# Performance work log

Hardware: AMD Instinct MI355X
Metric: run time of the kernel (lower is better)

The kernel has to match this reference:

```python
import jax, jax.numpy as jnp
import numpy as np

B, T, H, NH = 16, 2048, 1024, 16
HD = H // NH  # 64
IN0, IN1 = 256, 512  # modality input sizes needing projection; modality 2 is already H


def _ln(x, g, b, eps=1e-5):
    m = jnp.mean(x, axis=-1, keepdims=True)
    v = jnp.mean((x - m) ** 2, axis=-1, keepdims=True)
    return (x - m) / jnp.sqrt(v + eps) * g + b


def setup_inputs() -> dict:
    key = jax.random.key(0)
    ks = jax.random.split(key, 24)
    s = 0.02
    d = {
        'x0': jax.random.normal(ks[0], (B, T, IN0), jnp.float32),
        'x1': jax.random.normal(ks[1], (B, T, IN1), jnp.float32),
        'x2': jax.random.normal(ks[2], (B, T, H), jnp.float32),
        'static_context': jax.random.normal(ks[3], (B, T, H), jnp.float32),
        'Wp0': jax.random.normal(ks[4], (H, IN0), jnp.float32) * s,
        'bp0': jnp.zeros((H,), jnp.float32),
        'Wp1': jax.random.normal(ks[5], (H, IN1), jnp.float32) * s,
        'bp1': jnp.zeros((H,), jnp.float32),
        'Wq': jax.random.normal(ks[6], (H, H), jnp.float32) * s,
        'bq': jnp.zeros((H,), jnp.float32),
        'Wk': jax.random.normal(ks[7], (H, H), jnp.float32) * s,
        'bk': jnp.zeros((H,), jnp.float32),
        'Wv': jax.random.normal(ks[8], (H, H), jnp.float32) * s,
        'bv': jnp.zeros((H,), jnp.float32),
        'Wo': jax.random.normal(ks[9], (H, H), jnp.float32) * s,
        'bo': jnp.zeros((H,), jnp.float32),
        'query_token': jax.random.normal(ks[10], (H,), jnp.float32) * s,
        'g1': jnp.ones((H,), jnp.float32),
        'be1': jnp.zeros((H,), jnp.float32),
        'g2': jnp.ones((H,), jnp.float32),
        'be2': jnp.zeros((H,), jnp.float32),
        'W1': jax.random.normal(ks[11], (4 * H, H), jnp.float32) * s,
        'b1': jnp.zeros((4 * H,), jnp.float32),
        'W2': jax.random.normal(ks[12], (H, 4 * H), jnp.float32) * s,
        'b2': jnp.zeros((H,), jnp.float32),
    }
    return d


def _forward(x0, x1, x2, static_context, Wp0, bp0, Wp1, bp1, Wq, bq, Wk, bk, Wv, bv,
             Wo, bo, query_token, g1, be1, g2, be2, W1, b1, W2, b2):
    # project modalities to hidden size, stack -> [B, T, M, H]
    m0 = x0 @ Wp0.T + bp0
    m1 = x1 @ Wp1.T + bp1
    stacked = jnp.stack([m0, m1, x2], axis=2)  # [B,T,3,H]
    M = stacked.shape[2]
    # per-timestep single-query cross-attention over the M modality tokens,
    # batched over all B*T positions (equivalent to the torch per-t loop)
    q = query_token + static_context  # [B,T,H]
    Q = (q @ Wq.T + bq).reshape(B, T, NH, HD)
    K = (stacked @ Wk.T + bk).reshape(B, T, M, NH, HD)
    V = (stacked @ Wv.T + bv).reshape(B, T, M, NH, HD)
    scores = jnp.einsum('bthd,btmhd->bthm', Q, K) / jnp.sqrt(jnp.asarray(HD, Q.dtype))
    attn = jax.nn.softmax(scores, axis=-1)  # [B,T,NH,M]
    weights = attn.mean(axis=2)  # average over heads (torch default) -> [B,T,M]
    ctx = jnp.einsum('bthm,btmhd->bthd', attn, V).reshape(B, T, H)
    attn_out = ctx @ Wo.T + bo
    fused = _ln(attn_out, g1, be1)
    ff = jax.nn.gelu(fused @ W1.T + b1, approximate=False) @ W2.T + b2
    fused = _ln(fused + ff, g2, be2)
    return fused, weights


def reference(x0, x1, x2, static_context, Wp0, bp0, Wp1, bp1, Wq, bq, Wk, bk, Wv, bv,
              Wo, bo, query_token, g1, be1, g2, be2, W1, b1, W2, b2):
    return _forward(x0, x1, x2, static_context, Wp0, bp0, Wp1, bp1, Wq, bq, Wk, bk,
                    Wv, bv, Wo, bo, query_token, g1, be1, g2, be2, W1, b1, W2, b2)
```

## Files before the change

kernel.cpp:

```cpp
#include <hip/hip_runtime.h>
#include <hip/hip_bf16.h>
#include <math.h>

#define BT 32768
#define HH 1024

typedef unsigned short u16;
typedef __attribute__((ext_vector_type(4))) unsigned short u16x4;
typedef __attribute__((ext_vector_type(8))) __bf16 bf16x8;
typedef __attribute__((ext_vector_type(4))) float f32x4;

#define DEVI static __device__ __forceinline__

DEVI u16 f2bf(float f){
  unsigned u = __builtin_bit_cast(unsigned, f);
  u += 0x7FFFu + ((u >> 16) & 1u);
  return (u16)(u >> 16);
}
DEVI float bf2f(u16 h){
  unsigned u = ((unsigned)h) << 16;
  return __builtin_bit_cast(float, u);
}
DEVI void gl_lds16(const void* g, void* l){
  __builtin_amdgcn_global_load_lds((const __attribute__((address_space(1))) void*)g,
                                   (__attribute__((address_space(3))) void*)l, 16, 0, 0);
}
DEVI int swz(int row, int elem){ return elem ^ ((row & 7) << 3); }

__global__ void k_cast4(const float* __restrict__ s, u16* __restrict__ d, int n4){
  int i = blockIdx.x*blockDim.x + threadIdx.x;
  int st = gridDim.x*blockDim.x;
  for (; i < n4; i += st){
    float4 v = ((const float4*)s)[i];
    u16x4 o = { f2bf(v.x), f2bf(v.y), f2bf(v.z), f2bf(v.w) };
    ((u16x4*)d)[i] = o;
  }
}

__global__ void k_qb(const float* __restrict__ qt, const float* __restrict__ sc,
                     u16* __restrict__ d, int n4){
  int i = blockIdx.x*blockDim.x + threadIdx.x;
  int st = gridDim.x*blockDim.x;
  for (; i < n4; i += st){
    int e = i*4; int c = e & 1023;
    float4 v = *(const float4*)&sc[e];
    float4 q = *(const float4*)&qt[c];
    u16x4 o = { f2bf(v.x+q.x), f2bf(v.y+q.y), f2bf(v.z+q.z), f2bf(v.w+q.w) };
    ((u16x4*)d)[i] = o;
  }
}

__global__ void k_copyf(const float* __restrict__ s, float* __restrict__ d, int n){
  int i = blockIdx.x*blockDim.x + threadIdx.x;
  int st = gridDim.x*blockDim.x;
  for (; i < n; i += st) d[i] = s[i];
}

__global__ void k_transcast(const float* __restrict__ s, u16* __restrict__ d, int R, int C){
  __shared__ float tile[32][33];
  int c0 = blockIdx.x*32, r0 = blockIdx.y*32;
  int tx = threadIdx.x & 31, ty = threadIdx.x >> 5;
  #pragma unroll
  for (int i = 0; i < 32; i += 8) tile[ty+i][tx] = s[(size_t)(r0+ty+i)*C + c0+tx];
  __syncthreads();
  #pragma unroll
  for (int i = 0; i < 32; i += 8) d[(size_t)(c0+ty+i)*R + r0+tx] = f2bf(tile[tx][ty+i]);
}

__global__ void k_matvec(const u16* __restrict__ W, const float* __restrict__ x,
                         const float* __restrict__ badd, float* __restrict__ out, int K){
  int row = blockIdx.x*4 + (threadIdx.x>>6);
  int lane = threadIdx.x & 63;
  float s = 0.f;
  for (int k = lane; k < K; k += 64) s += bf2f(W[(size_t)row*K + k]) * x[k];
  #pragma unroll
  for (int m = 1; m < 64; m <<= 1) s += __shfl_xor(s, m);
  if (lane == 0) out[row] = s + badd[row];
}

__global__ __launch_bounds__(256, 3)
void k_gemm(const u16* __restrict__ A, int lda,
            const u16* __restrict__ B, int ldb, int K,
            const float* __restrict__ bias,
            u16* __restrict__ C, int ldc, int col0, int act)
{
  __shared__ u16 As[128*64];
  __shared__ u16 Bs[128*64];
  const int tid = threadIdx.x, lane = tid & 63, wid = tid >> 6;
  const int wr = wid >> 1, wc = wid & 1;
  const int r15 = lane & 15, g = lane >> 4;
  const int m0 = blockIdx.x * 128, n0 = blockIdx.y * 128;
  f32x4 acc[4][4] = {};

  for (int k0 = 0; k0 < K; k0 += 64){
    #pragma unroll
    for (int it = 0; it < 4; ++it){
      int c = it*256 + tid;
      int row = c >> 3;
      int ke = swz(row, (c & 7) * 8);
      gl_lds16(A + (size_t)(m0+row)*lda + (k0+ke), As + c*8);
      gl_lds16(B + (size_t)(n0+row)*ldb + (k0+ke), Bs + c*8);
    }
    __syncthreads();
    #pragma unroll
    for (int kk = 0; kk < 64; kk += 32){
      bf16x8 av[4], bvv[4];
      #pragma unroll
      for (int i = 0; i < 4; ++i){
        int row = wr*64 + i*16 + r15;
        av[i] = *(const bf16x8*)&As[row*64 + swz(row, kk + g*8)];
      }
      #pragma unroll
      for (int j = 0; j < 4; ++j){
        int row = wc*64 + j*16 + r15;
        bvv[j] = *(const bf16x8*)&Bs[row*64 + swz(row, kk + g*8)];
      }
      #pragma unroll
      for (int i = 0; i < 4; ++i)
        #pragma unroll
        for (int j = 0; j < 4; ++j)
          acc[i][j] = __builtin_amdgcn_mfma_f32_16x16x32_bf16(av[i], bvv[j], acc[i][j], 0, 0, 0);
    }
    __syncthreads();
  }
  #pragma unroll
  for (int j = 0; j < 4; ++j){
    int col = wc*64 + j*16 + r15;
    float bb = bias ? bias[n0 + col] : 0.f;
    #pragma unroll
    for (int i = 0; i < 4; ++i){
      #pragma unroll
      for (int jj = 0; jj < 4; ++jj){
        int row = wr*64 + i*16 + g*4 + jj;
        float v = acc[i][j][jj] + bb;
        if (act == 1) v = 0.5f * v * (1.f + erff(v * 0.70710678118654752f));
        C[(size_t)(m0+row)*ldc + col0 + n0 + col] = f2bf(v);
      }
    }
  }
}

__global__ __launch_bounds__(512, 2)
void k_gemm8(const u16* __restrict__ A, int lda,
             const u16* __restrict__ B, int ldb, int K,
             const float* __restrict__ bias,
             u16* __restrict__ C, int ldc, int act, int nn)
{
  __shared__ u16 As[2][2][128*64];
  __shared__ u16 Bs[2][2][128*64];
  const int tid = threadIdx.x, lane = tid & 63, wid = tid >> 6;
  const int wr = wid >> 2, wc = wid & 3;
  const int r15 = lane & 15, g = lane >> 4;
  const int cpx = gridDim.x >> 3;
  const int sid = ((int)blockIdx.x & 7) * cpx + ((int)blockIdx.x >> 3);
  const int m0 = (sid / nn) * 256, n0 = (sid % nn) * 256;
  const int nt = K >> 6;
  f32x4 acc[8][4] = {};
  const int srow = tid >> 3, scol = (tid & 7) * 8;

  auto stA = [&](int buf, int half, int t){
    int k0 = (t < nt ? t : nt-1) << 6;
    #pragma unroll
    for (int l = 0; l < 2; ++l){
      int lr = l*64 + srow;
      gl_lds16(A + (size_t)(m0 + half*128 + lr)*lda + k0 + swz(lr, scol),
               &As[buf][half][lr*64 + scol]);
    }
  };
  auto stB = [&](int buf, int half, int t){
    int k0 = (t < nt ? t : nt-1) << 6;
    #pragma unroll
    for (int l = 0; l < 2; ++l){
      int lr = l*64 + srow;
      gl_lds16(B + (size_t)(n0 + half*128 + lr)*ldb + k0 + swz(lr, scol),
               &Bs[buf][half][lr*64 + scol]);
    }
  };

  bf16x8 av[4][2], bv[2][2];
  auto loadq = [&](int buf, int MI, int NJ){
    #pragma unroll
    for (int i = 0; i < 4; ++i){
      int r = wr*64 + i*16 + r15;
      #pragma unroll
      for (int k2 = 0; k2 < 2; ++k2)
        av[i][k2] = *(const bf16x8*)&As[buf][MI][r*64 + swz(r, k2*32 + g*8)];
    }
    #pragma unroll
    for (int j = 0; j < 2; ++j){
      int cr = wc*32 + j*16 + r15;
      #pragma unroll
      for (int k2 = 0; k2 < 2; ++k2)
        bv[j][k2] = *(const bf16x8*)&Bs[buf][NJ][cr*64 + swz(cr, k2*32 + g*8)];
    }
  };
  auto mmaq = [&](int MI, int NJ){
    __builtin_amdgcn_s_setprio(1);
    #pragma unroll
    for (int k2 = 0; k2 < 2; ++k2)
      #pragma unroll
      for (int i = 0; i < 4; ++i)
        #pragma unroll
        for (int j = 0; j < 2; ++j)
          acc[MI*4+i][NJ*2+j] = __builtin_amdgcn_mfma_f32_16x16x32_bf16(
              av[i][k2], bv[j][k2], acc[MI*4+i][NJ*2+j], 0, 0, 0);
    __builtin_amdgcn_s_setprio(0);
  };

  stA(0,0,0); stA(0,1,0); stB(0,0,0); stB(0,1,0); stB(1,0,1); stA(1,0,1);
  asm volatile("s_waitcnt vmcnt(4)" ::: "memory");
  __builtin_amdgcn_s_barrier();

  for (int t = 0; t < nt; ++t){
    const int cur = t & 1, opp = cur ^ 1;
    loadq(cur, 0, 0);
    stA(opp, 1, t+1);
    mmaq(0, 0);
    asm volatile("s_waitcnt vmcnt(6) lgkmcnt(0)" ::: "memory");
    __builtin_amdgcn_s_barrier();
    loadq(cur, 1, 0);
    stB(opp, 1, t+1);
    mmaq(1, 0);
    asm volatile("s_waitcnt lgkmcnt(0)" ::: "memory");
    __builtin_amdgcn_s_barrier();
    loadq(cur, 0, 1);
    stB(cur, 0, t+2);
    mmaq(0, 1);
    asm volatile("s_waitcnt lgkmcnt(0)" ::: "memory");
    __builtin_amdgcn_s_barrier();
    loadq(cur, 1, 1);
    stA(cur, 0, t+2);
    mmaq(1, 1);
    asm volatile("s_waitcnt vmcnt(6) lgkmcnt(0)" ::: "memory");
    __builtin_amdgcn_s_barrier();
  }
  asm volatile("s_waitcnt vmcnt(0)" ::: "memory");

  #pragma unroll
  for (int jf = 0; jf < 4; ++jf){
    int col = n0 + (jf>>1)*128 + wc*32 + (jf&1)*16 + r15;
    float bb = bias ? bias[col] : 0.f;
    #pragma unroll
    for (int fi = 0; fi < 8; ++fi){
      #pragma unroll
      for (int jj = 0; jj < 4; ++jj){
        int row = m0 + (fi>>2)*128 + wr*64 + (fi&3)*16 + g*4 + jj;
        float v = acc[fi][jf][jj] + bb;
        if (act == 1) v = 0.5f * v * (1.f + erff(v * 0.70710678118654752f));
        C[(size_t)row*ldc + col] = f2bf(v);
      }
    }
  }
}

__global__ __launch_bounds__(512, 4)
void k_attn2p(const u16* __restrict__ x0b, const u16* __restrict__ x1b, const u16* __restrict__ x2b,
              const u16* __restrict__ Wc0, const u16* __restrict__ Wc1, const u16* __restrict__ Wc2,
              const float* __restrict__ bc0, const float* __restrict__ bc1, const float* __restrict__ bc2,
              const u16* __restrict__ Qg, u16* __restrict__ ctx, float* __restrict__ wacc)
{
  __shared__ __align__(16) u16 As[128*64];
  __shared__ __align__(16) u16 Bs[128*64];
  __shared__ float Sl[2*128*3];

  const int tid = threadIdx.x, lane = tid & 63, wid = tid >> 6;
  const int wr = wid >> 1, h = wid & 1;
  const int r15 = lane & 15, g = lane >> 4;
  const int bid = blockIdx.x;
  const int xcd = bid & 7;
  const int bn = (bid >> 3) & 7;
  const int btb = (bid >> 6) * 8 + xcd;
  const int t0 = btb * 128, n0 = bn * 128;

  const u16* Xs[3] = { x0b, x1b, x2b };
  const u16* Ws[3] = { Wc0, Wc1, Wc2 };
  const float* Bc[3] = { bc0, bc1, bc2 };
  const int Ks[3] = { 256, 512, 1024 };

  const int srow = tid >> 3;
  const int scol = (tid & 7) * 8;

  #pragma unroll
  for (int m = 0; m < 3; ++m){
    const int K = Ks[m];
    const u16* X = Xs[m];
    const u16* W = Ws[m];
    f32x4 aK[2][4] = {};
    for (int k0 = 0; k0 < K; k0 += 64){
      #pragma unroll
      for (int l = 0; l < 2; ++l){
        int row = l*64 + srow;
        int ke = swz(row, scol);
        gl_lds16(X + (size_t)(t0+row)*K + k0 + ke, &As[row*64 + scol]);
        gl_lds16(W + (size_t)(n0+row)*K + k0 + ke, &Bs[row*64 + scol]);
      }
      __syncthreads();
      #pragma unroll
      for (int kk = 0; kk < 64; kk += 32){
        bf16x8 av[2], bv[4];
        #pragma unroll
        for (int i = 0; i < 2; ++i){
          int ra = wr*32 + i*16 + r15;
          av[i] = *(const bf16x8*)&As[ra*64 + swz(ra, kk + g*8)];
        }
        #pragma unroll
        for (int j = 0; j < 4; ++j){
          int rb = h*64 + j*16 + r15;
          bv[j] = *(const bf16x8*)&Bs[rb*64 + swz(rb, kk + g*8)];
        }
        #pragma unroll
        for (int i = 0; i < 2; ++i)
          #pragma unroll
          for (int j = 0; j < 4; ++j)
            aK[i][j] = __builtin_amdgcn_mfma_f32_16x16x32_bf16(av[i], bv[j], aK[i][j], 0, 0, 0);
      }
      __syncthreads();
    }
    float bkc[4];
    #pragma unroll
    for (int j = 0; j < 4; ++j) bkc[j] = Bc[m][n0 + h*64 + j*16 + r15];
    #pragma unroll
    for (int i = 0; i < 2; ++i){
      #pragma unroll
      for (int jj = 0; jj < 4; ++jj){
        int tt = wr*32 + i*16 + g*4 + jj;
        const u16* qrow = Qg + (size_t)(t0+tt)*1024 + n0 + h*64 + r15;
        float s = 0.f;
        #pragma unroll
        for (int j = 0; j < 4; ++j)
          s += (aK[i][j][jj] + bkc[j]) * bf2f(qrow[j*16]);
        s += __shfl_xor(s, 1); s += __shfl_xor(s, 2);
        s += __shfl_xor(s, 4); s += __shfl_xor(s, 8);
        if (r15 == 0) Sl[(h*128 + tt)*3 + m] = s * 0.125f;
      }
    }
  }
  __syncthreads();
  if (tid < 256){
    int h2 = tid >> 7, tt = tid & 127;
    int base = (h2*128 + tt)*3;
    float s0 = Sl[base+0], s1 = Sl[base+1], s2 = Sl[base+2];
    float mx = fmaxf(s0, fmaxf(s1, s2));
    float e0 = expf(s0-mx), e1 = expf(s1-mx), e2 = expf(s2-mx);
    float inv = 1.f/(e0+e1+e2);
    e0 *= inv; e1 *= inv; e2 *= inv;
    Sl[base+0] = e0; Sl[base+1] = e1; Sl[base+2] = e2;
    atomicAdd(&wacc[(size_t)(t0+tt)*3 + 0], e0*0.0625f);
    atomicAdd(&wacc[(size_t)(t0+tt)*3 + 1], e1*0.0625f);
    atomicAdd(&wacc[(size_t)(t0+tt)*3 + 2], e2*0.0625f);
  }
  __syncthreads();

  f32x4 ctxa[2][4] = {};
  #pragma unroll
  for (int m = 0; m < 3; ++m){
    const int K = Ks[m];
    const u16* X = Xs[m];
    const u16* W = Ws[m] + (size_t)1024*K;
    f32x4 aV[2][4] = {};
    for (int k0 = 0; k0 < K; k0 += 64){
      #pragma unroll
      for (int l = 0; l < 2; ++l){
        int row = l*64 + srow;
        int ke = swz(row, scol);
        gl_lds16(X + (size_t)(t0+row)*K + k0 + ke, &As[row*64 + scol]);
        gl_lds16(W + (size_t)(n0+row)*K + k0 + ke, &Bs[row*64 + scol]);
      }
      __syncthreads();
      #pragma unroll
      for (int kk = 0; kk < 64; kk += 32){
        bf16x8 av[2], bv[4];
        #pragma unroll
        for (int i = 0; i < 2; ++i){
          int ra = wr*32 + i*16 + r15;
          av[i] = *(const bf16x8*)&As[ra*64 + swz(ra, kk + g*8)];
        }
        #pragma unroll
        for (int j = 0; j < 4; ++j){
          int rb = h*64 + j*16 + r15;
          bv[j] = *(const bf16x8*)&Bs[rb*64 + swz(rb, kk + g*8)];
        }
        #pragma unroll
        for (int i = 0; i < 2; ++i)
          #pragma unroll
          for (int j = 0; j < 4; ++j)
            aV[i][j] = __builtin_amdgcn_mfma_f32_16x16x32_bf16(av[i], bv[j], aV[i][j], 0, 0, 0);
      }
      __syncthreads();
    }
    #pragma unroll
    for (int j = 0; j < 4; ++j){
      float bvv = Bc[m][1024 + n0 + h*64 + j*16 + r15];
      #pragma unroll
      for (int i = 0; i < 2; ++i){
        #pragma unroll
        for (int jj = 0; jj < 4; ++jj){
          int tt = wr*32 + i*16 + g*4 + jj;
          float p = Sl[(h*128 + tt)*3 + m];
          ctxa[i][j][jj] += p * (aV[i][j][jj] + bvv);
        }
      }
    }
  }
  #pragma unroll
  for (int i = 0; i < 2; ++i){
    #pragma unroll
    for (int jj = 0; jj < 4; ++jj){
      int tt = wr*32 + i*16 + g*4 + jj;
      #pragma unroll
      for (int j = 0; j < 4; ++j)
        ctx[(size_t)(t0+tt)*1024 + n0 + h*64 + j*16 + r15] = f2bf(ctxa[i][j][jj]);
    }
  }
}

__global__ __launch_bounds__(256)
void k_ln(const u16* __restrict__ X, const u16* __restrict__ R,
          const float* __restrict__ gam, const float* __restrict__ bet,
          u16* __restrict__ outb, float* __restrict__ outf)
{
  __shared__ float rs[4], rq[4];
  const int t = blockIdx.x, tid = threadIdx.x;
  const size_t base = (size_t)t*1024 + tid*4;
  u16x4 xv = *(const u16x4*)&X[base];
  float v[4];
  #pragma unroll
  for (int i = 0; i < 4; ++i) v[i] = bf2f(xv[i]);
  if (R){
    u16x4 rv = *(const u16x4*)&R[base];
    #pragma unroll
    for (int i = 0; i < 4; ++i) v[i] += bf2f(rv[i]);
  }
  float s = v[0]+v[1]+v[2]+v[3];
  float q = v[0]*v[0]+v[1]*v[1]+v[2]*v[2]+v[3]*v[3];
  #pragma unroll
  for (int m = 1; m < 64; m <<= 1){ s += __shfl_xor(s, m); q += __shfl_xor(q, m); }
  if ((tid & 63) == 0){ rs[tid>>6] = s; rq[tid>>6] = q; }
  __syncthreads();
  s = rs[0]+rs[1]+rs[2]+rs[3];
  q = rq[0]+rq[1]+rq[2]+rq[3];
  float mean = s * (1.f/1024.f);
  float var  = q * (1.f/1024.f) - mean*mean;
  float rstd = rsqrtf(var + 1e-5f);
  int c0 = tid*4;
  if (outb){
    u16x4 o;
    #pragma unroll
    for (int i = 0; i < 4; ++i) o[i] = f2bf((v[i]-mean)*rstd*gam[c0+i] + bet[c0+i]);
    *(u16x4*)&outb[base] = o;
  } else {
    float4 o;
    o.x = (v[0]-mean)*rstd*gam[c0+0] + bet[c0+0];
    o.y = (v[1]-mean)*rstd*gam[c0+1] + bet[c0+1];
    o.z = (v[2]-mean)*rstd*gam[c0+2] + bet[c0+2];
    o.w = (v[3]-mean)*rstd*gam[c0+3] + bet[c0+3];
    *(float4*)&outf[base] = o;
  }
}

extern "C" void kernel_launch(void* const* d_in, const int* in_sizes, int n_in,
                              void* d_out, int out_size, void* d_ws, size_t ws_size,
                              hipStream_t stream)
{
  (void)in_sizes; (void)n_in; (void)out_size;
  const float* x0  = (const float*)d_in[0];
  const float* x1  = (const float*)d_in[1];
  const float* x2  = (const float*)d_in[2];
  const float* sc  = (const float*)d_in[3];
  const float* Wp0 = (const float*)d_in[4];  const float* bp0 = (const float*)d_in[5];
  const float* Wp1 = (const float*)d_in[6];  const float* bp1 = (const float*)d_in[7];
  const float* Wq  = (const float*)d_in[8];  const float* bq  = (const float*)d_in[9];
  const float* Wk  = (const float*)d_in[10]; const float* bk  = (const float*)d_in[11];
  const float* Wv  = (const float*)d_in[12]; const float* bv  = (const float*)d_in[13];
  const float* Wo  = (const float*)d_in[14]; const float* bo  = (const float*)d_in[15];
  const float* qt  = (const float*)d_in[16];
  const float* g1  = (const float*)d_in[17]; const float* be1 = (const float*)d_in[18];
  const float* g2  = (const float*)d_in[19]; const float* be2 = (const float*)d_in[20];
  const float* W1  = (const float*)d_in[21]; const float* b1  = (const float*)d_in[22];
  const float* W2  = (const float*)d_in[23]; const float* b2  = (const float*)d_in[24];

  char* ws = (char*)d_ws;
  size_t off = 0;
  auto alloc = [&](size_t b)->char*{ char* p = ws + off; off += (b + 255) & ~(size_t)255; return p; };

  u16* Wqb   = (u16*)alloc((size_t)1024*1024*2);
  u16* Wob   = (u16*)alloc((size_t)1024*1024*2);
  u16* W1b   = (u16*)alloc((size_t)4096*1024*2);
  u16* W2b   = (u16*)alloc((size_t)1024*4096*2);
  u16* Wkvb  = (u16*)alloc((size_t)2048*1024*2);
  u16* Wp0t  = (u16*)alloc((size_t)256*1024*2);
  u16* Wp1t  = (u16*)alloc((size_t)512*1024*2);
  u16* Wkv0c = (u16*)alloc((size_t)2048*256*2);
  u16* Wkv1c = (u16*)alloc((size_t)2048*512*2);
  float* bc0 = (float*)alloc((size_t)2048*4);
  float* bc1 = (float*)alloc((size_t)2048*4);
  float* bc2 = (float*)alloc((size_t)2048*4);
  char* regX  = alloc((size_t)BT*(256+512+1024)*2);
  char* regQ1 = alloc((size_t)BT*1024*2);
  char* regQ2 = alloc((size_t)BT*1024*2);
  float* wacc = (float*)alloc((size_t)BT*3*4);
  if (off > ws_size) return;
  u16* ff1big = nullptr;
  if (off + (size_t)16384*4096*2 <= ws_size) ff1big = (u16*)alloc((size_t)16384*4096*2);

  u16* x0b = (u16*)regX;
  u16* x1b = (u16*)(regX + (size_t)BT*256*2);
  u16* x2b = (u16*)(regX + (size_t)BT*768*2);
  u16* aob  = (u16*)regX;
  u16* ff2b = (u16*)regX;
  u16* qb   = (u16*)regQ1;
  u16* ctxb = (u16*)regQ1;
  u16* f1b  = (u16*)regQ1;
  u16* Qb   = (u16*)regQ2;

  hipMemsetAsync(wacc, 0, (size_t)BT*3*4, stream);

  dim3 B256(256), B512(512);
  auto cast4 = [&](const float* s, u16* d, int n, int grid){
    k_cast4<<<dim3(grid), B256, 0, stream>>>(s, d, n >> 2);
  };
  cast4(Wq, Wqb, 1024*1024, 1024);
  cast4(Wk, Wkvb, 1024*1024, 1024);
  cast4(Wv, Wkvb + (size_t)1024*1024, 1024*1024, 1024);
  cast4(Wo, Wob, 1024*1024, 1024);
  cast4(W1, W1b, 4096*1024, 1024);
  cast4(W2, W2b, 4096*1024, 1024);
  cast4(x0, x0b, BT*256, 1024);
  cast4(x1, x1b, BT*512, 1024);
  cast4(x2, x2b, BT*1024, 2048);
  k_transcast<<<dim3(8, 32),  B256, 0, stream>>>(Wp0, Wp0t, 1024, 256);
  k_transcast<<<dim3(16, 32), B256, 0, stream>>>(Wp1, Wp1t, 1024, 512);
  k_copyf<<<dim3(4), B256, 0, stream>>>(bk, bc2, 1024);
  k_copyf<<<dim3(4), B256, 0, stream>>>(bv, bc2 + 1024, 1024);
  k_matvec<<<dim3(512), B256, 0, stream>>>(Wkvb, bp0, bc2, bc0, 1024);
  k_matvec<<<dim3(512), B256, 0, stream>>>(Wkvb, bp1, bc2, bc1, 1024);
  k_qb<<<dim3(2048), B256, 0, stream>>>(qt, sc, qb, BT*256);

  k_gemm<<<dim3(16, 2), B256, 0, stream>>>(Wkvb, 1024, Wp0t, 1024, 1024, nullptr, Wkv0c, 256, 0, 0);
  k_gemm<<<dim3(16, 4), B256, 0, stream>>>(Wkvb, 1024, Wp1t, 1024, 1024, nullptr, Wkv1c, 512, 0, 0);

  k_gemm8<<<dim3(512), B512, 0, stream>>>(qb, 1024, Wqb, 1024, 1024, bq, Qb, 1024, 0, 4);
  k_attn2p<<<dim3(BT/128*8), B512, 0, stream>>>(x0b, x1b, x2b, Wkv0c, Wkv1c, Wkvb,
                                                bc0, bc1, bc2, Qb, ctxb, wacc);
  k_gemm8<<<dim3(512), B512, 0, stream>>>(ctxb, 1024, Wob, 1024, 1024, bo, aob, 1024, 0, 4);
  k_ln<<<dim3(BT), B256, 0, stream>>>(aob, nullptr, g1, be1, f1b, nullptr);

  if (ff1big){
    for (int c = 0; c < 2; ++c){
      const u16* fa = f1b + (size_t)c*16384*1024;
      k_gemm8<<<dim3(1024), B512, 0, stream>>>(fa, 1024, W1b, 1024, 1024, b1, ff1big, 4096, 1, 16);
      k_gemm8<<<dim3(256),  B512, 0, stream>>>(ff1big, 4096, W2b, 4096, 4096, b2,
                                               ff2b + (size_t)c*16384*1024, 1024, 0, 4);
    }
  } else {
    u16* ff1c = (u16*)regQ2;
    for (int c = 0; c < 4; ++c){
      const u16* fa = f1b + (size_t)c*8192*1024;
      k_gemm8<<<dim3(512), B512, 0, stream>>>(fa, 1024, W1b, 1024, 1024, b1, ff1c, 4096, 1, 16);
      k_gemm8<<<dim3(128), B512, 0, stream>>>(ff1c, 4096, W2b, 4096, 4096, b2,
                                              ff2b + (size_t)c*8192*1024, 1024, 0, 4);
    }
  }
  float* outf = (float*)d_out;
  k_ln<<<dim3(BT), B256, 0, stream>>>(ff2b, f1b, g2, be2, nullptr, outf);
  k_copyf<<<dim3(384), B256, 0, stream>>>(wacc, outf + (size_t)BT*1024, BT*3);
}
```

Baseline: 1.695 ms.

## Fuse K/V passes in attention, defer head-weight softmax, reschedule FFN GEMM barriers

The attention kernel now computes K and V projections in a single pass over the inputs with 64-row tiles, using an unnormalized exp-weighted context (no max subtraction) instead of two passes with a shared softmax. Per-head scores go to a buffer and a new kernel computes the head-averaged weights, which removes the atomics and the memset. The FFN GEMM gets sched_barrier fences and moves its s_barrier ahead of each MFMA group. The Q and O projections switch from the 256-tile GEMM to the smaller k_gemm, which could be slower on those GEMMs. Skipping max subtraction risks overflow for large scores.

```diff
diff --git a/kernel.cpp b/kernel.cpp
--- a/kernel.cpp
+++ b/kernel.cpp
@@ -7,6 +7,7 @@
 
 typedef unsigned short u16;
 typedef __attribute__((ext_vector_type(4))) unsigned short u16x4;
+typedef __attribute__((ext_vector_type(8))) unsigned short u16x8;
 typedef __attribute__((ext_vector_type(8))) __bf16 bf16x8;
 typedef __attribute__((ext_vector_type(4))) float f32x4;
 
@@ -54,6 +55,26 @@
   int i = blockIdx.x*blockDim.x + threadIdx.x;
   int st = gridDim.x*blockDim.x;
   for (; i < n; i += st) d[i] = s[i];
+}
+
+__global__ void k_wsm(const float* __restrict__ s, float* __restrict__ out, int T){
+  int t = blockIdx.x*blockDim.x + threadIdx.x;
+  int st = gridDim.x*blockDim.x;
+  for (; t < T; t += st){
+    float a0 = 0.f, a1 = 0.f, a2 = 0.f;
+    #pragma unroll
+    for (int h = 0; h < 16; ++h){
+      const float* b = s + (size_t)t*48 + h*3;
+      float s0 = b[0], s1 = b[1], s2 = b[2];
+      float mx = fmaxf(s0, fmaxf(s1, s2));
+      float e0 = __expf(s0-mx), e1 = __expf(s1-mx), e2 = __expf(s2-mx);
+      float inv = 1.f/(e0+e1+e2);
+      a0 += e0*inv; a1 += e1*inv; a2 += e2*inv;
+    }
+    out[(size_t)t*3+0] = a0*0.0625f;
+    out[(size_t)t*3+1] = a1*0.0625f;
+    out[(size_t)t*3+2] = a2*0.0625f;
+  }
 }
 
 __global__ void k_transcast(const float* __restrict__ s, u16* __restrict__ d, int R, int C){
@@ -141,10 +162,10 @@
 }
 
 __global__ __launch_bounds__(512, 2)
-void k_gemm8(const u16* __restrict__ A, int lda,
-             const u16* __restrict__ B, int ldb, int K,
-             const float* __restrict__ bias,
-             u16* __restrict__ C, int ldc, int act, int nn)
+void k_gemm8x(const u16* __restrict__ A, int lda,
+              const u16* __restrict__ B, int ldb, int K,
+              const float* __restrict__ bias,
+              u16* __restrict__ C, int ldc, int act, int nn)
 {
   __shared__ u16 As[2][2][128*64];
   __shared__ u16 Bs[2][2][128*64];
@@ -210,29 +231,46 @@
   stA(0,0,0); stA(0,1,0); stB(0,0,0); stB(0,1,0); stB(1,0,1); stA(1,0,1);
   asm volatile("s_waitcnt vmcnt(4)" ::: "memory");
   __builtin_amdgcn_s_barrier();
+  __builtin_amdgcn_sched_barrier(0);
 
   for (int t = 0; t < nt; ++t){
     const int cur = t & 1, opp = cur ^ 1;
     loadq(cur, 0, 0);
     stA(opp, 1, t+1);
+    __builtin_amdgcn_sched_barrier(0);
+    __builtin_amdgcn_s_barrier();
+    asm volatile("s_waitcnt vmcnt(6) lgkmcnt(0)" ::: "memory");
+    __builtin_amdgcn_sched_barrier(0);
     mmaq(0, 0);
-    asm volatile("s_waitcnt vmcnt(6) lgkmcnt(0)" ::: "memory");
-    __builtin_amdgcn_s_barrier();
+    __builtin_amdgcn_s_barrier();
+    __builtin_amdgcn_sched_barrier(0);
     loadq(cur, 1, 0);
     stB(opp, 1, t+1);
+    __builtin_amdgcn_sched_barrier(0);
+    __builtin_amdgcn_s_barrier();
+    asm volatile("s_waitcnt lgkmcnt(0)" ::: "memory");
+    __builtin_amdgcn_sched_barrier(0);
     mmaq(1, 0);
-    asm volatile("s_waitcnt lgkmcnt(0)" ::: "memory");
-    __builtin_amdgcn_s_barrier();
+    __builtin_amdgcn_s_barrier();
+    __builtin_amdgcn_sched_barrier(0);
     loadq(cur, 0, 1);
     stB(cur, 0, t+2);
+    __builtin_amdgcn_sched_barrier(0);
+    __builtin_amdgcn_s_barrier();
+    asm volatile("s_waitcnt lgkmcnt(0)" ::: "memory");
+    __builtin_amdgcn_sched_barrier(0);
     mmaq(0, 1);
-    asm volatile("s_waitcnt lgkmcnt(0)" ::: "memory");
-    __builtin_amdgcn_s_barrier();
+    __builtin_amdgcn_s_barrier();
+    __builtin_amdgcn_sched_barrier(0);
     loadq(cur, 1, 1);
     stA(cur, 0, t+2);
+    __builtin_amdgcn_sched_barrier(0);
+    __builtin_amdgcn_s_barrier();
+    asm volatile("s_waitcnt vmcnt(6) lgkmcnt(0)" ::: "memory");
+    __builtin_amdgcn_sched_barrier(0);
     mmaq(1, 1);
-    asm volatile("s_waitcnt vmcnt(6) lgkmcnt(0)" ::: "memory");
-    __builtin_amdgcn_s_barrier();
+    __builtin_amdgcn_s_barrier();
+    __builtin_amdgcn_sched_barrier(0);
   }
   asm volatile("s_waitcnt vmcnt(0)" ::: "memory");
 
@@ -254,163 +292,94 @@
 }
 
 __global__ __launch_bounds__(512, 4)
-void k_attn2p(const u16* __restrict__ x0b, const u16* __restrict__ x1b, const u16* __restrict__ x2b,
+void k_attn1p(const u16* __restrict__ x0b, const u16* __restrict__ x1b, const u16* __restrict__ x2b,
               const u16* __restrict__ Wc0, const u16* __restrict__ Wc1, const u16* __restrict__ Wc2,
               const float* __restrict__ bc0, const float* __restrict__ bc1, const float* __restrict__ bc2,
-              const u16* __restrict__ Qg, u16* __restrict__ ctx, float* __restrict__ wacc)
+              const u16* __restrict__ Qg, u16* __restrict__ ctx, float* __restrict__ sbuf)
 {
-  __shared__ __align__(16) u16 As[128*64];
-  __shared__ __align__(16) u16 Bs[128*64];
-  __shared__ float Sl[2*128*3];
+  __shared__ __align__(16) u16 As[64*64];
+  __shared__ __align__(16) u16 Bk[128*64];
+  __shared__ __align__(16) u16 Bv[128*64];
 
   const int tid = threadIdx.x, lane = tid & 63, wid = tid >> 6;
   const int wr = wid >> 1, h = wid & 1;
   const int r15 = lane & 15, g = lane >> 4;
   const int bid = blockIdx.x;
-  const int xcd = bid & 7;
-  const int bn = (bid >> 3) & 7;
-  const int btb = (bid >> 6) * 8 + xcd;
-  const int t0 = btb * 128, n0 = bn * 128;
+  const int xcd = bid & 7, bn = (bid >> 3) & 7, btb = (bid >> 6) * 8 + xcd;
+  const int t0 = btb * 64, n0 = bn * 128;
+  const int arow = tid >> 3, acol = (tid & 7) * 8;
 
   const u16* Xs[3] = { x0b, x1b, x2b };
   const u16* Ws[3] = { Wc0, Wc1, Wc2 };
   const float* Bc[3] = { bc0, bc1, bc2 };
   const int Ks[3] = { 256, 512, 1024 };
 
-  const int srow = tid >> 3;
-  const int scol = (tid & 7) * 8;
+  f32x4 cx[4] = {};
+  float dn[4] = {0.f, 0.f, 0.f, 0.f};
 
   #pragma unroll
   for (int m = 0; m < 3; ++m){
     const int K = Ks[m];
-    const u16* X = Xs[m];
-    const u16* W = Ws[m];
-    f32x4 aK[2][4] = {};
+    const u16* X  = Xs[m];
+    const u16* WK = Ws[m];
+    const u16* WV = Ws[m] + (size_t)1024*K;
+    f32x4 aK[4] = {}, aV[4] = {};
     for (int k0 = 0; k0 < K; k0 += 64){
+      gl_lds16(X + (size_t)(t0+arow)*K + k0 + swz(arow, acol), &As[arow*64 + acol]);
       #pragma unroll
       for (int l = 0; l < 2; ++l){
-        int row = l*64 + srow;
-        int ke = swz(row, scol);
-        gl_lds16(X + (size_t)(t0+row)*K + k0 + ke, &As[row*64 + scol]);
-        gl_lds16(W + (size_t)(n0+row)*K + k0 + ke, &Bs[row*64 + scol]);
+        int row = l*64 + arow;
+        gl_lds16(WK + (size_t)(n0+row)*K + k0 + swz(row, acol), &Bk[row*64 + acol]);
+        gl_lds16(WV + (size_t)(n0+row)*K + k0 + swz(row, acol), &Bv[row*64 + acol]);
       }
       __syncthreads();
       #pragma unroll
-      for (int kk = 0; kk < 64; kk += 32){
-        bf16x8 av[2], bv[4];
-        #pragma unroll
-        for (int i = 0; i < 2; ++i){
-          int ra = wr*32 + i*16 + r15;
-          av[i] = *(const bf16x8*)&As[ra*64 + swz(ra, kk + g*8)];
-        }
+      for (int k2 = 0; k2 < 2; ++k2){
+        int ra = wr*16 + r15;
+        bf16x8 a2 = *(const bf16x8*)&As[ra*64 + swz(ra, k2*32 + g*8)];
         #pragma unroll
         for (int j = 0; j < 4; ++j){
           int rb = h*64 + j*16 + r15;
-          bv[j] = *(const bf16x8*)&Bs[rb*64 + swz(rb, kk + g*8)];
+          bf16x8 kb = *(const bf16x8*)&Bk[rb*64 + swz(rb, k2*32 + g*8)];
+          bf16x8 vb = *(const bf16x8*)&Bv[rb*64 + swz(rb, k2*32 + g*8)];
+          aK[j] = __builtin_amdgcn_mfma_f32_16x16x32_bf16(a2, kb, aK[j], 0, 0, 0);
+          aV[j] = __builtin_amdgcn_mfma_f32_16x16x32_bf16(a2, vb, aV[j], 0, 0, 0);
         }
-        #pragma unroll
-        for (int i = 0; i < 2; ++i)
-          #pragma unroll
-          for (int j = 0; j < 4; ++j)
-            aK[i][j] = __builtin_amdgcn_mfma_f32_16x16x32_bf16(av[i], bv[j], aK[i][j], 0, 0, 0);
       }
       __syncthreads();
     }
-    float bkc[4];
-    #pragma unroll
-    for (int j = 0; j < 4; ++j) bkc[j] = Bc[m][n0 + h*64 + j*16 + r15];
-    #pragma unroll
-    for (int i = 0; i < 2; ++i){
-      #pragma unroll
-      for (int jj = 0; jj < 4; ++jj){
-        int tt = wr*32 + i*16 + g*4 + jj;
-        const u16* qrow = Qg + (size_t)(t0+tt)*1024 + n0 + h*64 + r15;
-        float s = 0.f;
-        #pragma unroll
-        for (int j = 0; j < 4; ++j)
-          s += (aK[i][j][jj] + bkc[j]) * bf2f(qrow[j*16]);
-        s += __shfl_xor(s, 1); s += __shfl_xor(s, 2);
-        s += __shfl_xor(s, 4); s += __shfl_xor(s, 8);
-        if (r15 == 0) Sl[(h*128 + tt)*3 + m] = s * 0.125f;
-      }
-    }
-  }
-  __syncthreads();
-  if (tid < 256){
-    int h2 = tid >> 7, tt = tid & 127;
-    int base = (h2*128 + tt)*3;
-    float s0 = Sl[base+0], s1 = Sl[base+1], s2 = Sl[base+2];
-    float mx = fmaxf(s0, fmaxf(s1, s2));
-    float e0 = expf(s0-mx), e1 = expf(s1-mx), e2 = expf(s2-mx);
-    float inv = 1.f/(e0+e1+e2);
-    e0 *= inv; e1 *= inv; e2 *= inv;
-    Sl[base+0] = e0; Sl[base+1] = e1; Sl[base+2] = e2;
-    atomicAdd(&wacc[(size_t)(t0+tt)*3 + 0], e0*0.0625f);
-    atomicAdd(&wacc[(size_t)(t0+tt)*3 + 1], e1*0.0625f);
-    atomicAdd(&wacc[(size_t)(t0+tt)*3 + 2], e2*0.0625f);
-  }
-  __syncthreads();
-
-  f32x4 ctxa[2][4] = {};
-  #pragma unroll
-  for (int m = 0; m < 3; ++m){
-    const int K = Ks[m];
-    const u16* X = Xs[m];
-    const u16* W = Ws[m] + (size_t)1024*K;
-    f32x4 aV[2][4] = {};
-    for (int k0 = 0; k0 < K; k0 += 64){
-      #pragma unroll
-      for (int l = 0; l < 2; ++l){
-        int row = l*64 + srow;
-        int ke = swz(row, scol);
-        gl_lds16(X + (size_t)(t0+row)*K + k0 + ke, &As[row*64 + scol]);
-        gl_lds16(W + (size_t)(n0+row)*K + k0 + ke, &Bs[row*64 + scol]);
-      }
-      __syncthreads();
-      #pragma unroll
-      for (int kk = 0; kk < 64; kk += 32){
-        bf16x8 av[2], bv[4];
-        #pragma unroll
-        for (int i = 0; i < 2; ++i){
-          int ra = wr*32 + i*16 + r15;
-          av[i] = *(const bf16x8*)&As[ra*64 + swz(ra, kk + g*8)];
-        }
-        #pragma unroll
-        for (int j = 0; j < 4; ++j){
-          int rb = h*64 + j*16 + r15;
-          bv[j] = *(const bf16x8*)&Bs[rb*64 + swz(rb, kk + g*8)];
-        }
-        #pragma unroll
-        for (int i = 0; i < 2; ++i)
-          #pragma unroll
-          for (int j = 0; j < 4; ++j)
-            aV[i][j] = __builtin_amdgcn_mfma_f32_16x16x32_bf16(av[i], bv[j], aV[i][j], 0, 0, 0);
-      }
-      __syncthreads();
-    }
+    float bkc[4], bvc[4];
     #pragma unroll
     for (int j = 0; j < 4; ++j){
-      float bvv = Bc[m][1024 + n0 + h*64 + j*16 + r15];
-      #pragma unroll
-      for (int i = 0; i < 2; ++i){
-        #pragma unroll
-        for (int jj = 0; jj < 4; ++jj){
-          int tt = wr*32 + i*16 + g*4 + jj;
-          float p = Sl[(h*128 + tt)*3 + m];
-          ctxa[i][j][jj] += p * (aV[i][j][jj] + bvv);
-        }
-      }
-    }
-  }
-  #pragma unroll
-  for (int i = 0; i < 2; ++i){
+      bkc[j] = Bc[m][n0 + h*64 + j*16 + r15];
+      bvc[j] = Bc[m][1024 + n0 + h*64 + j*16 + r15];
+    }
     #pragma unroll
     for (int jj = 0; jj < 4; ++jj){
-      int tt = wr*32 + i*16 + g*4 + jj;
+      int tt = wr*16 + g*4 + jj;
+      const u16* qrow = Qg + (size_t)(t0+tt)*1024 + n0 + h*64 + r15;
+      float s = 0.f;
       #pragma unroll
       for (int j = 0; j < 4; ++j)
-        ctx[(size_t)(t0+tt)*1024 + n0 + h*64 + j*16 + r15] = f2bf(ctxa[i][j][jj]);
-    }
+        s += (aK[j][jj] + bkc[j]) * bf2f(qrow[j*16]);
+      s += __shfl_xor(s, 1); s += __shfl_xor(s, 2);
+      s += __shfl_xor(s, 4); s += __shfl_xor(s, 8);
+      s *= 0.125f;
+      if (r15 == 0) sbuf[((size_t)(t0+tt)*16 + bn*2 + h)*3 + m] = s;
+      float e = __expf(s);
+      dn[jj] += e;
+      #pragma unroll
+      for (int j = 0; j < 4; ++j)
+        cx[j][jj] += e * (aV[j][jj] + bvc[j]);
+    }
+  }
+  #pragma unroll
+  for (int jj = 0; jj < 4; ++jj){
+    float inv = 1.f / dn[jj];
+    int tt = wr*16 + g*4 + jj;
+    #pragma unroll
+    for (int j = 0; j < 4; ++j)
+      ctx[(size_t)(t0+tt)*1024 + n0 + h*64 + j*16 + r15] = f2bf(cx[j][jj] * inv);
   }
 }
 
@@ -498,7 +467,7 @@
   char* regX  = alloc((size_t)BT*(256+512+1024)*2);
   char* regQ1 = alloc((size_t)BT*1024*2);
   char* regQ2 = alloc((size_t)BT*1024*2);
-  float* wacc = (float*)alloc((size_t)BT*3*4);
+  float* sbuf = (float*)alloc((size_t)BT*48*4);
   if (off > ws_size) return;
   u16* ff1big = nullptr;
   if (off + (size_t)16384*4096*2 <= ws_size) ff1big = (u16*)alloc((size_t)16384*4096*2);
@@ -512,8 +481,6 @@
   u16* ctxb = (u16*)regQ1;
   u16* f1b  = (u16*)regQ1;
   u16* Qb   = (u16*)regQ2;
-
-  hipMemsetAsync(wacc, 0, (size_t)BT*3*4, stream);
 
   dim3 B256(256), B512(512);
   auto cast4 = [&](const float* s, u16* d, int n, int grid){
@@ -539,29 +506,29 @@
   k_gemm<<<dim3(16, 2), B256, 0, stream>>>(Wkvb, 1024, Wp0t, 1024, 1024, nullptr, Wkv0c, 256, 0, 0);
   k_gemm<<<dim3(16, 4), B256, 0, stream>>>(Wkvb, 1024, Wp1t, 1024, 1024, nullptr, Wkv1c, 512, 0, 0);
 
-  k_gemm8<<<dim3(512), B512, 0, stream>>>(qb, 1024, Wqb, 1024, 1024, bq, Qb, 1024, 0, 4);
-  k_attn2p<<<dim3(BT/128*8), B512, 0, stream>>>(x0b, x1b, x2b, Wkv0c, Wkv1c, Wkvb,
-                                                bc0, bc1, bc2, Qb, ctxb, wacc);
-  k_gemm8<<<dim3(512), B512, 0, stream>>>(ctxb, 1024, Wob, 1024, 1024, bo, aob, 1024, 0, 4);
+  k_gemm<<<dim3(BT/128, 8), B256, 0, stream>>>(qb, 1024, Wqb, 1024, 1024, bq, Qb, 1024, 0, 0);
+  k_attn1p<<<dim3(BT/64*8), B512, 0, stream>>>(x0b, x1b, x2b, Wkv0c, Wkv1c, Wkvb,
+                                               bc0, bc1, bc2, Qb, ctxb, sbuf);
+  k_gemm<<<dim3(BT/128, 8), B256, 0, stream>>>(ctxb, 1024, Wob, 1024, 1024, bo, aob, 1024, 0, 0);
   k_ln<<<dim3(BT), B256, 0, stream>>>(aob, nullptr, g1, be1, f1b, nullptr);
 
   if (ff1big){
     for (int c = 0; c < 2; ++c){
       const u16* fa = f1b + (size_t)c*16384*1024;
-      k_gemm8<<<dim3(1024), B512, 0, stream>>>(fa, 1024, W1b, 1024, 1024, b1, ff1big, 4096, 1, 16);
-      k_gemm8<<<dim3(256),  B512, 0, stream>>>(ff1big, 4096, W2b, 4096, 4096, b2,
-                                               ff2b + (size_t)c*16384*1024, 1024, 0, 4);
+      k_gemm8x<<<dim3(1024), B512, 0, stream>>>(fa, 1024, W1b, 1024, 1024, b1, ff1big, 4096, 1, 16);
+      k_gemm8x<<<dim3(256),  B512, 0, stream>>>(ff1big, 4096, W2b, 4096, 4096, b2,
+                                                ff2b + (size_t)c*16384*1024, 1024, 0, 4);
     }
   } else {
     u16* ff1c = (u16*)regQ2;
     for (int c = 0; c < 4; ++c){
       const u16* fa = f1b + (size_t)c*8192*1024;
-      k_gemm8<<<dim3(512), B512, 0, stream>>>(fa, 1024, W1b, 1024, 1024, b1, ff1c, 4096, 1, 16);
-      k_gemm8<<<dim3(128), B512, 0, stream>>>(ff1c, 4096, W2b, 4096, 4096, b2,
-                                              ff2b + (size_t)c*8192*1024, 1024, 0, 4);
+      k_gemm8x<<<dim3(512), B512, 0, stream>>>(fa, 1024, W1b, 1024, 1024, b1, ff1c, 4096, 1, 16);
+      k_gemm8x<<<dim3(128), B512, 0, stream>>>(ff1c, 4096, W2b, 4096, 4096, b2,
+                                               ff2b + (size_t)c*8192*1024, 1024, 0, 4);
     }
   }
   float* outf = (float*)d_out;
   k_ln<<<dim3(BT), B256, 0, stream>>>(ff2b, f1b, g2, be2, nullptr, outf);
-  k_copyf<<<dim3(384), B256, 0, stream>>>(wacc, outf + (size_t)BT*1024, BT*3);
-}
+  k_wsm<<<dim3(128), B256, 0, stream>>>(sbuf, outf + (size_t)BT*1024, BT);
+}
```

Measured after the change: 1.720 ms. No clear change (+1.5%).
